# Kernel optimization log

Hardware: AMD Instinct MI355X
Metric: run time of the kernel (lower is better)

## Reference

```python
import jax, jax.numpy as jnp
import numpy as np
import math

EMBED = 512
KDIM = 512
VDIM = 512
H = 8
HD = EMBED // H
N = 2048
L = 2048
B = 4


def setup_inputs() -> dict:
    key = jax.random.key(0)
    ks = jax.random.split(key, 14)
    s = 1.0 / math.sqrt(EMBED)
    return {
        "q": jax.random.normal(ks[0], (N, B, EMBED), jnp.float32),
        "k": jax.random.normal(ks[1], (L, B, KDIM), jnp.float32),
        "v": jax.random.normal(ks[2], (L, B, VDIM), jnp.float32),
        "pe1": jax.random.normal(ks[3], (B, N, 3), jnp.float32),
        "pe2": jax.random.normal(ks[4], (L, 3), jnp.float32),
        "Wq": jax.random.normal(ks[5], (EMBED, EMBED), jnp.float32) * s,
        "bq": jnp.zeros((EMBED,), jnp.float32),
        "Wk": jax.random.normal(ks[6], (EMBED, KDIM), jnp.float32) * s,
        "bk": jnp.zeros((EMBED,), jnp.float32),
        "Wv": jax.random.normal(ks[7], (EMBED, VDIM), jnp.float32) * s,
        "bv": jnp.zeros((EMBED,), jnp.float32),
        "Wo": jax.random.normal(ks[8], (EMBED, EMBED), jnp.float32) * s,
        "bo": jnp.zeros((EMBED,), jnp.float32),
    }


def reference(q, k, v, pe1, pe2, Wq, bq, Wk, bk, Wv, bv, Wo, bo):
    n, b, _ = q.shape
    l = k.shape[0]
    # projections (nn.Linear: x @ W.T + b)
    qp = q @ Wq.T + bq  # (n, b, E)
    kp = k @ Wk.T + bk  # (l, b, E)
    vp = v @ Wv.T + bv  # (l, b, E)
    # split heads -> (b, H, n, hd)
    qh = qp.reshape(n, b, H, HD).transpose(1, 2, 0, 3)
    kh = kp.reshape(l, b, H, HD).transpose(1, 2, 0, 3)
    vh = vp.reshape(l, b, H, HD).transpose(1, 2, 0, 3)
    # relative PE bias: (b, n, l), broadcast over heads
    pe_scores = jnp.einsum('bnc,lc->bnl', pe1, pe2)[:, None, :, :]
    scores = (jnp.einsum('bhnd,bhld->bhnl', qh, kh) + pe_scores) / math.sqrt(HD)
    attn = jax.nn.softmax(scores, axis=-1)
    out = jnp.einsum('bhnl,bhld->bhnd', attn, vh)  # (b, H, n, hd)
    out = out.transpose(2, 0, 1, 3).reshape(n, b, EMBED)
    return out @ Wo.T + bo
```

## Files before the change

kernel.cpp:

```cpp
#include <hip/hip_runtime.h>
#include <math.h>

#define EMBED 512
#define HDIM 64
#define NHEADS 8
#define SEQ_N 2048
#define SEQ_L 2048
#define BATCH 4
#define MROWS (SEQ_N*BATCH)
#define BE (BATCH*EMBED)

#define QSCALE 0.18033688f

typedef _Float16 f16;
typedef _Float16 half8 __attribute__((ext_vector_type(8)));
typedef _Float16 half4 __attribute__((ext_vector_type(4)));
typedef float floatx4 __attribute__((ext_vector_type(4)));
typedef float floatx16 __attribute__((ext_vector_type(16)));

static __device__ inline float fast_exp2(float x) {
#if __has_builtin(__builtin_amdgcn_exp2f)
  return __builtin_amdgcn_exp2f(x);
#else
  return __expf(x * 0.69314718056f);
#endif
}

__global__ __launch_bounds__(256) void cvt_all(const float* __restrict__ q,
                                               const float* __restrict__ k,
                                               const float* __restrict__ v,
                                               const float* __restrict__ Wq,
                                               const float* __restrict__ Wk,
                                               const float* __restrict__ Wv,
                                               const float* __restrict__ Wo,
                                               f16* __restrict__ qb, f16* __restrict__ kb,
                                               f16* __restrict__ vb, f16* __restrict__ Wb) {
  const long TOK = (long)MROWS * EMBED;
  const long WSZ = (long)EMBED * EMBED;
  int y = blockIdx.y;
  long i = ((long)blockIdx.x * 256 + threadIdx.x) * 4;
  if (y < 3) {
    if (i < TOK) {
      const float* s = y == 0 ? q : y == 1 ? k : v;
      f16* d = y == 0 ? qb : y == 1 ? kb : vb;
      float4 f = *reinterpret_cast<const float4*>(s + i);
      half4 o; o[0] = (f16)f.x; o[1] = (f16)f.y; o[2] = (f16)f.z; o[3] = (f16)f.w;
      *reinterpret_cast<half4*>(d + i) = o;
    }
  } else {
    if (i < 4 * WSZ) {
      int sel = (int)(i >> 18);
      long off = i & (WSZ - 1);
      const float* s = sel == 0 ? Wq : sel == 1 ? Wk : sel == 2 ? Wv : Wo;
      float4 f = *reinterpret_cast<const float4*>(s + off);
      half4 o; o[0] = (f16)f.x; o[1] = (f16)f.y; o[2] = (f16)f.z; o[3] = (f16)f.w;
      *reinterpret_cast<half4*>(Wb + i) = o;
    }
  }
}

__global__ __launch_bounds__(256) void gemm_qkv(const f16* __restrict__ A0,
                                                const f16* __restrict__ A1,
                                                const f16* __restrict__ A2,
                                                const f16* __restrict__ W0,
                                                const f16* __restrict__ W1,
                                                const f16* __restrict__ W2,
                                                const float* __restrict__ b0,
                                                const float* __restrict__ b1,
                                                const float* __restrict__ b2,
                                                f16* __restrict__ C0, f16* __restrict__ C1,
                                                f16* __restrict__ C2t) {
  __shared__ alignas(16) f16 As[128 * 40];
  __shared__ alignas(16) f16 Bs[128 * 40];
  const int sel = blockIdx.y >> 2;
  const f16* A = sel == 0 ? A0 : sel == 1 ? A1 : A2;
  const f16* Bt = sel == 0 ? W0 : sel == 1 ? W1 : W2;
  const float* bias = sel == 0 ? b0 : sel == 1 ? b1 : b2;
  const float scl = sel == 0 ? QSCALE : 1.0f;
  const int tid = threadIdx.x;
  const int wave = tid >> 6, lane = tid & 63, quad = lane >> 4, l16 = lane & 15;
  const int wm = wave & 1, wn = wave >> 1;
  const long m0 = (long)blockIdx.x * 128;
  const long n0 = (long)(blockIdx.y & 3) * 128;
  floatx4 acc[4][4] = {};
  const int r0 = tid >> 2;
  const int c0 = (tid & 3) * 8;

  for (int k0 = 0; k0 < EMBED; k0 += 32) {
    __syncthreads();
    uint4 a0 = *reinterpret_cast<const uint4*>(A + (m0 + r0) * EMBED + k0 + c0);
    uint4 a1 = *reinterpret_cast<const uint4*>(A + (m0 + r0 + 64) * EMBED + k0 + c0);
    uint4 bb0 = *reinterpret_cast<const uint4*>(Bt + (n0 + r0) * EMBED + k0 + c0);
    uint4 bb1 = *reinterpret_cast<const uint4*>(Bt + (n0 + r0 + 64) * EMBED + k0 + c0);
    *reinterpret_cast<uint4*>(&As[r0 * 40 + c0]) = a0;
    *reinterpret_cast<uint4*>(&As[(r0 + 64) * 40 + c0]) = a1;
    *reinterpret_cast<uint4*>(&Bs[r0 * 40 + c0]) = bb0;
    *reinterpret_cast<uint4*>(&Bs[(r0 + 64) * 40 + c0]) = bb1;
    __syncthreads();
    half8 af[4], bf[4];
#pragma unroll
    for (int i = 0; i < 4; ++i)
      af[i] = *reinterpret_cast<const half8*>(&As[(wm * 64 + i * 16 + l16) * 40 + quad * 8]);
#pragma unroll
    for (int j = 0; j < 4; ++j)
      bf[j] = *reinterpret_cast<const half8*>(&Bs[(wn * 64 + j * 16 + l16) * 40 + quad * 8]);
#pragma unroll
    for (int i = 0; i < 4; ++i)
#pragma unroll
      for (int j = 0; j < 4; ++j)
        acc[i][j] = __builtin_amdgcn_mfma_f32_16x16x32_f16(af[i], bf[j], acc[i][j], 0, 0, 0);
  }
#pragma unroll
  for (int i = 0; i < 4; ++i)
#pragma unroll
    for (int r = 0; r < 4; ++r) {
      long row = m0 + wm * 64 + i * 16 + quad * 4 + r;
#pragma unroll
      for (int j = 0; j < 4; ++j) {
        long col = n0 + wn * 64 + j * 16 + l16;
        float val = (acc[i][j][r] + bias[col]) * scl;
        if (sel == 2) {
          long bq = row & 3, ltok = row >> 2;
          long hh = col >> 6, dd = col & 63;
          C2t[(((bq << 3) + hh) * 64 + dd) * 2048 + ltok] = (f16)val;
        } else {
          f16* C = sel == 0 ? C0 : C1;
          C[row * EMBED + col] = (f16)val;
        }
      }
    }
}

__global__ __launch_bounds__(256) void gemm_out(const f16* __restrict__ A,
                                                const f16* __restrict__ Bt,
                                                const float* __restrict__ bias,
                                                float* __restrict__ C) {
  __shared__ alignas(16) f16 As[128 * 40];
  __shared__ alignas(16) f16 Bs[64 * 40];
  const int tid = threadIdx.x;
  const int wave = tid >> 6, lane = tid & 63, quad = lane >> 4, l16 = lane & 15;
  const long m0 = (long)blockIdx.x * 128;
  const long n0 = (long)blockIdx.y * 64;
  floatx4 acc[2][4] = {};
  const int r0 = tid >> 2;
  const int c0 = (tid & 3) * 8;

  for (int k0 = 0; k0 < EMBED; k0 += 32) {
    __syncthreads();
    uint4 a0 = *reinterpret_cast<const uint4*>(A + (m0 + r0) * EMBED + k0 + c0);
    uint4 a1 = *reinterpret_cast<const uint4*>(A + (m0 + r0 + 64) * EMBED + k0 + c0);
    uint4 bb0 = *reinterpret_cast<const uint4*>(Bt + (n0 + r0) * EMBED + k0 + c0);
    *reinterpret_cast<uint4*>(&As[r0 * 40 + c0]) = a0;
    *reinterpret_cast<uint4*>(&As[(r0 + 64) * 40 + c0]) = a1;
    *reinterpret_cast<uint4*>(&Bs[r0 * 40 + c0]) = bb0;
    __syncthreads();
    half8 af[2], bf[4];
#pragma unroll
    for (int i = 0; i < 2; ++i)
      af[i] = *reinterpret_cast<const half8*>(&As[(wave * 32 + i * 16 + l16) * 40 + quad * 8]);
#pragma unroll
    for (int j = 0; j < 4; ++j)
      bf[j] = *reinterpret_cast<const half8*>(&Bs[(j * 16 + l16) * 40 + quad * 8]);
#pragma unroll
    for (int i = 0; i < 2; ++i)
#pragma unroll
      for (int j = 0; j < 4; ++j)
        acc[i][j] = __builtin_amdgcn_mfma_f32_16x16x32_f16(af[i], bf[j], acc[i][j], 0, 0, 0);
  }
#pragma unroll
  for (int i = 0; i < 2; ++i)
#pragma unroll
    for (int r = 0; r < 4; ++r) {
      long row = m0 + wave * 32 + i * 16 + quad * 4 + r;
#pragma unroll
      for (int j = 0; j < 4; ++j) {
        long col = n0 + j * 16 + l16;
        C[row * EMBED + col] = acc[i][j][r] + bias[col];
      }
    }
}

#define KST 88
#define VST 136
__global__ __launch_bounds__(256, 2) void attn_flash(const f16* __restrict__ qp,
                                                     const f16* __restrict__ kp,
                                                     const f16* __restrict__ vt,
                                                     const float* __restrict__ pe1,
                                                     const float* __restrict__ pe2,
                                                     f16* __restrict__ ao) {
  __shared__ alignas(16) f16 Qs[128 * KST];
  __shared__ alignas(16) f16 Ks[128 * KST];
  __shared__ alignas(16) f16 Vt[64 * VST];
  const int tid = threadIdx.x, wave = tid >> 6, lane = tid & 63;
  const int m = lane & 31, h = lane >> 5;
  const int n0 = blockIdx.x * 128;
  const int b = blockIdx.y >> 3, hd = blockIdx.y & 7;
  const long headoff = (long)b * EMBED + hd * HDIM;
  const long vhead = (long)blockIdx.y * 64 * 2048;

  for (int c = tid; c < 1024; c += 256) {
    int r = c >> 3, col = (c & 7) * 8;
    *reinterpret_cast<uint4*>(&Qs[r * KST + col]) =
        *reinterpret_cast<const uint4*>(qp + (long)(n0 + r) * BE + headoff + col);
  }
  const uint4 z4 = {0, 0, 0, 0};
  const uint2 z2 = {0, 0};
  for (int c = tid; c < 512; c += 256) {
    int r = c >> 2, s = c & 3;
    if (s == 0) *reinterpret_cast<uint2*>(&Qs[r * KST + 68]) = z2;
    else if (s == 1) *reinterpret_cast<uint4*>(&Qs[r * KST + 72]) = z4;
    else if (s == 2) *reinterpret_cast<uint4*>(&Qs[r * KST + 80]) = z4;
    if (s == 0) *reinterpret_cast<uint2*>(&Ks[r * KST + 68]) = z2;
    else if (s == 1) *reinterpret_cast<uint4*>(&Ks[r * KST + 72]) = z4;
    else if (s == 2) *reinterpret_cast<uint4*>(&Ks[r * KST + 80]) = z4;
  }
  if (tid < 128) {
    long base = ((long)b * SEQ_N + n0 + tid) * 3;
    half4 v8;
    v8[0] = (f16)(pe1[base + 0] * QSCALE);
    v8[1] = (f16)(pe1[base + 1] * QSCALE);
    v8[2] = (f16)(pe1[base + 2] * QSCALE);
    v8[3] = (f16)0.f;
    *reinterpret_cast<half4*>(&Qs[tid * KST + 64]) = v8;
  }
  __syncthreads();

  half8 qf[5];
#pragma unroll
  for (int e = 0; e < 5; ++e)
    qf[e] = *reinterpret_cast<const half8*>(&Qs[(wave * 32 + m) * KST + e * 16 + h * 8]);

  floatx16 oacc[2] = {};
  float lpart = 0.f;

  for (int l0 = 0; l0 < SEQ_L; l0 += 128) {
    __syncthreads();
    for (int c = tid; c < 1024; c += 256) {
      int r = c >> 3, col = (c & 7) * 8;
      *reinterpret_cast<uint4*>(&Ks[r * KST + col]) =
          *reinterpret_cast<const uint4*>(kp + (long)(l0 + r) * BE + headoff + col);
    }
    for (int c = tid; c < 1024; c += 256) {
      int r = c >> 4, col = (c & 15) * 8;
      *reinterpret_cast<uint4*>(&Vt[r * VST + col]) =
          *reinterpret_cast<const uint4*>(vt + vhead + (long)r * 2048 + l0 + col);
    }
    if (tid < 128) {
      long bb = (long)(l0 + tid) * 3;
      half4 p2;
      p2[0] = (f16)pe2[bb + 0];
      p2[1] = (f16)pe2[bb + 1];
      p2[2] = (f16)pe2[bb + 2];
      p2[3] = (f16)0.f;
      *reinterpret_cast<half4*>(&Ks[tid * KST + 64]) = p2;
    }
    __syncthreads();

#pragma unroll
    for (int t = 0; t < 4; ++t) {
      floatx16 st = {};
#pragma unroll
      for (int e = 0; e < 5; ++e) {
        half8 kf = *reinterpret_cast<const half8*>(&Ks[(t * 32 + m) * KST + e * 16 + h * 8]);
        st = __builtin_amdgcn_mfma_f32_32x32x16_f16(kf, qf[e], st, 0, 0, 0);
      }
      float p[16];
#pragma unroll
      for (int r = 0; r < 16; ++r) {
        p[r] = fast_exp2(st[r]);
        lpart += p[r];
      }
#pragma unroll
      for (int s = 0; s < 4; ++s) {
        half4 bp;
        bp[0] = (f16)p[4 * s + 0];
        bp[1] = (f16)p[4 * s + 1];
        bp[2] = (f16)p[4 * s + 2];
        bp[3] = (f16)p[4 * s + 3];
        int lcol = t * 32 + s * 8 + h * 4;
#pragma unroll
        for (int dt = 0; dt < 2; ++dt) {
          half4 vf = *reinterpret_cast<const half4*>(&Vt[(dt * 32 + m) * VST + lcol]);
          oacc[dt] = __builtin_amdgcn_mfma_f32_32x32x8f16(vf, bp, oacc[dt], 0, 0, 0);
        }
      }
    }
  }

  lpart += __shfl_xor(lpart, 32);
  float inv = 1.f / lpart;
  long qrow = n0 + wave * 32 + m;
#pragma unroll
  for (int dt = 0; dt < 2; ++dt)
#pragma unroll
    for (int g = 0; g < 4; ++g) {
      half4 o4;
      o4[0] = (f16)(oacc[dt][4 * g + 0] * inv);
      o4[1] = (f16)(oacc[dt][4 * g + 1] * inv);
      o4[2] = (f16)(oacc[dt][4 * g + 2] * inv);
      o4[3] = (f16)(oacc[dt][4 * g + 3] * inv);
      int d = dt * 32 + 8 * g + 4 * h;
      *reinterpret_cast<half4*>(ao + qrow * BE + headoff + d) = o4;
    }
}

extern "C" void kernel_launch(void* const* d_in, const int* in_sizes, int n_in,
                              void* d_out, int out_size, void* d_ws, size_t ws_size,
                              hipStream_t stream) {
  const float* q   = (const float*)d_in[0];
  const float* k   = (const float*)d_in[1];
  const float* v   = (const float*)d_in[2];
  const float* pe1 = (const float*)d_in[3];
  const float* pe2 = (const float*)d_in[4];
  const float* Wq  = (const float*)d_in[5];
  const float* bq  = (const float*)d_in[6];
  const float* Wk  = (const float*)d_in[7];
  const float* bk  = (const float*)d_in[8];
  const float* Wv  = (const float*)d_in[9];
  const float* bv  = (const float*)d_in[10];
  const float* Wo  = (const float*)d_in[11];
  const float* bo  = (const float*)d_in[12];
  float* out = (float*)d_out;

  f16* ws = (f16*)d_ws;
  const long TOK = (long)MROWS * EMBED;
  const long WSZ = (long)EMBED * EMBED;
  f16* qb  = ws;
  f16* kb  = qb + TOK;
  f16* vb  = kb + TOK;
  f16* Wqb = vb + TOK;
  f16* Wkb = Wqb + WSZ;
  f16* Wvb = Wkb + WSZ;
  f16* Wob = Wvb + WSZ;
  f16* qpb = Wob + WSZ;
  f16* kpb = qpb + TOK;
  f16* vtb = kpb + TOK;
  f16* aob = vtb + TOK;

  cvt_all<<<dim3(4096, 4), 256, 0, stream>>>(q, k, v, Wq, Wk, Wv, Wo, qb, kb, vb, Wqb);

  gemm_qkv<<<dim3(MROWS / 128, 12), 256, 0, stream>>>(qb, kb, vb, Wqb, Wkb, Wvb,
                                                      bq, bk, bv, qpb, kpb, vtb);

  attn_flash<<<dim3(SEQ_N / 128, BATCH * NHEADS), 256, 0, stream>>>(qpb, kpb, vtb, pe1, pe2, aob);

  gemm_out<<<dim3(MROWS / 128, EMBED / 64), 256, 0, stream>>>(aob, Wob, bo, out);
}
```

Baseline: 228.4 us.

## Fuse fp32-to-fp16 conversion into GEMM loads and prefetch K/V chunks in attention

Removes the separate conversion kernel. The QKV and output GEMMs now load fp32 inputs and weights directly and pack them to fp16 with cvt_pkrtz while staging into LDS, which saves one launch and a full write plus re-read of the converted tensors. The attention kernel register-prefetches the next K/V/pe2 chunk during compute (software pipelining), splits the output accumulators and the row-sum into two interleaved chains, and packs the probabilities with pkrtz. In exchange the GEMMs read twice the bytes per tile from global memory and repeat the conversion across tiles, the prefetch registers raise register pressure, and round-toward-zero conversion slightly changes numerics.

```diff
diff --git a/kernel.cpp b/kernel.cpp
--- a/kernel.cpp
+++ b/kernel.cpp
@@ -15,6 +15,7 @@
 typedef _Float16 f16;
 typedef _Float16 half8 __attribute__((ext_vector_type(8)));
 typedef _Float16 half4 __attribute__((ext_vector_type(4)));
+typedef _Float16 half2v __attribute__((ext_vector_type(2)));
 typedef float floatx4 __attribute__((ext_vector_type(4)));
 typedef float floatx16 __attribute__((ext_vector_type(16)));
 
@@ -26,45 +27,29 @@
 #endif
 }
 
-__global__ __launch_bounds__(256) void cvt_all(const float* __restrict__ q,
-                                               const float* __restrict__ k,
-                                               const float* __restrict__ v,
-                                               const float* __restrict__ Wq,
-                                               const float* __restrict__ Wk,
-                                               const float* __restrict__ Wv,
-                                               const float* __restrict__ Wo,
-                                               f16* __restrict__ qb, f16* __restrict__ kb,
-                                               f16* __restrict__ vb, f16* __restrict__ Wb) {
-  const long TOK = (long)MROWS * EMBED;
-  const long WSZ = (long)EMBED * EMBED;
-  int y = blockIdx.y;
-  long i = ((long)blockIdx.x * 256 + threadIdx.x) * 4;
-  if (y < 3) {
-    if (i < TOK) {
-      const float* s = y == 0 ? q : y == 1 ? k : v;
-      f16* d = y == 0 ? qb : y == 1 ? kb : vb;
-      float4 f = *reinterpret_cast<const float4*>(s + i);
-      half4 o; o[0] = (f16)f.x; o[1] = (f16)f.y; o[2] = (f16)f.z; o[3] = (f16)f.w;
-      *reinterpret_cast<half4*>(d + i) = o;
-    }
-  } else {
-    if (i < 4 * WSZ) {
-      int sel = (int)(i >> 18);
-      long off = i & (WSZ - 1);
-      const float* s = sel == 0 ? Wq : sel == 1 ? Wk : sel == 2 ? Wv : Wo;
-      float4 f = *reinterpret_cast<const float4*>(s + off);
-      half4 o; o[0] = (f16)f.x; o[1] = (f16)f.y; o[2] = (f16)f.z; o[3] = (f16)f.w;
-      *reinterpret_cast<half4*>(Wb + i) = o;
-    }
-  }
-}
-
-__global__ __launch_bounds__(256) void gemm_qkv(const f16* __restrict__ A0,
-                                                const f16* __restrict__ A1,
-                                                const f16* __restrict__ A2,
-                                                const f16* __restrict__ W0,
-                                                const f16* __restrict__ W1,
-                                                const f16* __restrict__ W2,
+static __device__ inline half2v pk2(float a, float b) {
+#if __has_builtin(__builtin_amdgcn_cvt_pkrtz)
+  return __builtin_bit_cast(half2v, __builtin_amdgcn_cvt_pkrtz(a, b));
+#else
+  half2v o; o[0] = (f16)a; o[1] = (f16)b; return o;
+#endif
+}
+
+static __device__ inline half8 cvt8(const float4& a, const float4& b) {
+  half2v p0 = pk2(a.x, a.y), p1 = pk2(a.z, a.w);
+  half2v p2 = pk2(b.x, b.y), p3 = pk2(b.z, b.w);
+  half8 o;
+  o[0] = p0[0]; o[1] = p0[1]; o[2] = p1[0]; o[3] = p1[1];
+  o[4] = p2[0]; o[5] = p2[1]; o[6] = p3[0]; o[7] = p3[1];
+  return o;
+}
+
+__global__ __launch_bounds__(256) void gemm_qkv(const float* __restrict__ A0,
+                                                const float* __restrict__ A1,
+                                                const float* __restrict__ A2,
+                                                const float* __restrict__ W0,
+                                                const float* __restrict__ W1,
+                                                const float* __restrict__ W2,
                                                 const float* __restrict__ b0,
                                                 const float* __restrict__ b1,
                                                 const float* __restrict__ b2,
@@ -73,8 +58,8 @@
   __shared__ alignas(16) f16 As[128 * 40];
   __shared__ alignas(16) f16 Bs[128 * 40];
   const int sel = blockIdx.y >> 2;
-  const f16* A = sel == 0 ? A0 : sel == 1 ? A1 : A2;
-  const f16* Bt = sel == 0 ? W0 : sel == 1 ? W1 : W2;
+  const float* A = sel == 0 ? A0 : sel == 1 ? A1 : A2;
+  const float* Bt = sel == 0 ? W0 : sel == 1 ? W1 : W2;
   const float* bias = sel == 0 ? b0 : sel == 1 ? b1 : b2;
   const float scl = sel == 0 ? QSCALE : 1.0f;
   const int tid = threadIdx.x;
@@ -88,14 +73,18 @@
 
   for (int k0 = 0; k0 < EMBED; k0 += 32) {
     __syncthreads();
-    uint4 a0 = *reinterpret_cast<const uint4*>(A + (m0 + r0) * EMBED + k0 + c0);
-    uint4 a1 = *reinterpret_cast<const uint4*>(A + (m0 + r0 + 64) * EMBED + k0 + c0);
-    uint4 bb0 = *reinterpret_cast<const uint4*>(Bt + (n0 + r0) * EMBED + k0 + c0);
-    uint4 bb1 = *reinterpret_cast<const uint4*>(Bt + (n0 + r0 + 64) * EMBED + k0 + c0);
-    *reinterpret_cast<uint4*>(&As[r0 * 40 + c0]) = a0;
-    *reinterpret_cast<uint4*>(&As[(r0 + 64) * 40 + c0]) = a1;
-    *reinterpret_cast<uint4*>(&Bs[r0 * 40 + c0]) = bb0;
-    *reinterpret_cast<uint4*>(&Bs[(r0 + 64) * 40 + c0]) = bb1;
+    float4 a00 = *reinterpret_cast<const float4*>(A + (m0 + r0) * EMBED + k0 + c0);
+    float4 a01 = *reinterpret_cast<const float4*>(A + (m0 + r0) * EMBED + k0 + c0 + 4);
+    float4 a10 = *reinterpret_cast<const float4*>(A + (m0 + r0 + 64) * EMBED + k0 + c0);
+    float4 a11 = *reinterpret_cast<const float4*>(A + (m0 + r0 + 64) * EMBED + k0 + c0 + 4);
+    float4 w00 = *reinterpret_cast<const float4*>(Bt + (n0 + r0) * EMBED + k0 + c0);
+    float4 w01 = *reinterpret_cast<const float4*>(Bt + (n0 + r0) * EMBED + k0 + c0 + 4);
+    float4 w10 = *reinterpret_cast<const float4*>(Bt + (n0 + r0 + 64) * EMBED + k0 + c0);
+    float4 w11 = *reinterpret_cast<const float4*>(Bt + (n0 + r0 + 64) * EMBED + k0 + c0 + 4);
+    *reinterpret_cast<half8*>(&As[r0 * 40 + c0]) = cvt8(a00, a01);
+    *reinterpret_cast<half8*>(&As[(r0 + 64) * 40 + c0]) = cvt8(a10, a11);
+    *reinterpret_cast<half8*>(&Bs[r0 * 40 + c0]) = cvt8(w00, w01);
+    *reinterpret_cast<half8*>(&Bs[(r0 + 64) * 40 + c0]) = cvt8(w10, w11);
     __syncthreads();
     half8 af[4], bf[4];
 #pragma unroll
@@ -132,7 +121,7 @@
 }
 
 __global__ __launch_bounds__(256) void gemm_out(const f16* __restrict__ A,
-                                                const f16* __restrict__ Bt,
+                                                const float* __restrict__ Wt,
                                                 const float* __restrict__ bias,
                                                 float* __restrict__ C) {
   __shared__ alignas(16) f16 As[128 * 40];
@@ -149,10 +138,11 @@
     __syncthreads();
     uint4 a0 = *reinterpret_cast<const uint4*>(A + (m0 + r0) * EMBED + k0 + c0);
     uint4 a1 = *reinterpret_cast<const uint4*>(A + (m0 + r0 + 64) * EMBED + k0 + c0);
-    uint4 bb0 = *reinterpret_cast<const uint4*>(Bt + (n0 + r0) * EMBED + k0 + c0);
+    float4 w0 = *reinterpret_cast<const float4*>(Wt + (n0 + r0) * EMBED + k0 + c0);
+    float4 w1 = *reinterpret_cast<const float4*>(Wt + (n0 + r0) * EMBED + k0 + c0 + 4);
     *reinterpret_cast<uint4*>(&As[r0 * 40 + c0]) = a0;
     *reinterpret_cast<uint4*>(&As[(r0 + 64) * 40 + c0]) = a1;
-    *reinterpret_cast<uint4*>(&Bs[r0 * 40 + c0]) = bb0;
+    *reinterpret_cast<half8*>(&Bs[r0 * 40 + c0]) = cvt8(w0, w1);
     __syncthreads();
     half8 af[2], bf[4];
 #pragma unroll
@@ -182,6 +172,7 @@
 
 #define KST 88
 #define VST 136
+#define NCHUNK (SEQ_L / 128)
 __global__ __launch_bounds__(256, 2) void attn_flash(const f16* __restrict__ qp,
                                                      const f16* __restrict__ kp,
                                                      const f16* __restrict__ vt,
@@ -223,39 +214,54 @@
     v8[3] = (f16)0.f;
     *reinterpret_cast<half4*>(&Qs[tid * KST + 64]) = v8;
   }
+
+  uint4 kr[4], vr[4];
+  float p2a = 0.f, p2b = 0.f, p2c = 0.f;
+  auto load_chunk = [&](int l0) {
+#pragma unroll
+    for (int i = 0; i < 4; ++i) {
+      int idx = tid + i * 256;
+      int r = idx >> 3, col = (idx & 7) * 8;
+      kr[i] = *reinterpret_cast<const uint4*>(kp + (long)(l0 + r) * BE + headoff + col);
+      int rv = idx >> 4, cv = (idx & 15) * 8;
+      vr[i] = *reinterpret_cast<const uint4*>(vt + vhead + (long)rv * 2048 + l0 + cv);
+    }
+    if (tid < 128) {
+      long bb = (long)(l0 + tid) * 3;
+      p2a = pe2[bb + 0]; p2b = pe2[bb + 1]; p2c = pe2[bb + 2];
+    }
+  };
+  auto store_chunk = [&]() {
+#pragma unroll
+    for (int i = 0; i < 4; ++i) {
+      int idx = tid + i * 256;
+      int r = idx >> 3, col = (idx & 7) * 8;
+      *reinterpret_cast<uint4*>(&Ks[r * KST + col]) = kr[i];
+      int rv = idx >> 4, cv = (idx & 15) * 8;
+      *reinterpret_cast<uint4*>(&Vt[rv * VST + cv]) = vr[i];
+    }
+    if (tid < 128) {
+      half4 p2;
+      p2[0] = (f16)p2a; p2[1] = (f16)p2b; p2[2] = (f16)p2c; p2[3] = (f16)0.f;
+      *reinterpret_cast<half4*>(&Ks[tid * KST + 64]) = p2;
+    }
+  };
+
+  load_chunk(0);
   __syncthreads();
-
   half8 qf[5];
 #pragma unroll
   for (int e = 0; e < 5; ++e)
     qf[e] = *reinterpret_cast<const half8*>(&Qs[(wave * 32 + m) * KST + e * 16 + h * 8]);
-
-  floatx16 oacc[2] = {};
-  float lpart = 0.f;
-
-  for (int l0 = 0; l0 < SEQ_L; l0 += 128) {
-    __syncthreads();
-    for (int c = tid; c < 1024; c += 256) {
-      int r = c >> 3, col = (c & 7) * 8;
-      *reinterpret_cast<uint4*>(&Ks[r * KST + col]) =
-          *reinterpret_cast<const uint4*>(kp + (long)(l0 + r) * BE + headoff + col);
-    }
-    for (int c = tid; c < 1024; c += 256) {
-      int r = c >> 4, col = (c & 15) * 8;
-      *reinterpret_cast<uint4*>(&Vt[r * VST + col]) =
-          *reinterpret_cast<const uint4*>(vt + vhead + (long)r * 2048 + l0 + col);
-    }
-    if (tid < 128) {
-      long bb = (long)(l0 + tid) * 3;
-      half4 p2;
-      p2[0] = (f16)pe2[bb + 0];
-      p2[1] = (f16)pe2[bb + 1];
-      p2[2] = (f16)pe2[bb + 2];
-      p2[3] = (f16)0.f;
-      *reinterpret_cast<half4*>(&Ks[tid * KST + 64]) = p2;
-    }
-    __syncthreads();
-
+  store_chunk();
+
+  floatx16 oacc[2][2] = {};
+  float lp0 = 0.f, lp1 = 0.f;
+
+#pragma unroll 1
+  for (int c = 0; c < NCHUNK; ++c) {
+    if (c + 1 < NCHUNK) load_chunk((c + 1) * 128);
+    __syncthreads();
 #pragma unroll
     for (int t = 0; t < 4; ++t) {
       floatx16 st = {};
@@ -266,27 +272,30 @@
       }
       float p[16];
 #pragma unroll
-      for (int r = 0; r < 16; ++r) {
-        p[r] = fast_exp2(st[r]);
-        lpart += p[r];
-      }
+      for (int r = 0; r < 16; ++r) p[r] = fast_exp2(st[r]);
+#pragma unroll
+      for (int r = 0; r < 16; r += 2) { lp0 += p[r]; lp1 += p[r + 1]; }
 #pragma unroll
       for (int s = 0; s < 4; ++s) {
+        half2v u0 = pk2(p[4 * s + 0], p[4 * s + 1]);
+        half2v u1 = pk2(p[4 * s + 2], p[4 * s + 3]);
         half4 bp;
-        bp[0] = (f16)p[4 * s + 0];
-        bp[1] = (f16)p[4 * s + 1];
-        bp[2] = (f16)p[4 * s + 2];
-        bp[3] = (f16)p[4 * s + 3];
+        bp[0] = u0[0]; bp[1] = u0[1]; bp[2] = u1[0]; bp[3] = u1[1];
         int lcol = t * 32 + s * 8 + h * 4;
 #pragma unroll
         for (int dt = 0; dt < 2; ++dt) {
           half4 vf = *reinterpret_cast<const half4*>(&Vt[(dt * 32 + m) * VST + lcol]);
-          oacc[dt] = __builtin_amdgcn_mfma_f32_32x32x8f16(vf, bp, oacc[dt], 0, 0, 0);
+          oacc[dt][t & 1] = __builtin_amdgcn_mfma_f32_32x32x8f16(vf, bp, oacc[dt][t & 1], 0, 0, 0);
         }
       }
     }
-  }
-
+    if (c + 1 < NCHUNK) {
+      __syncthreads();
+      store_chunk();
+    }
+  }
+
+  float lpart = lp0 + lp1;
   lpart += __shfl_xor(lpart, 32);
   float inv = 1.f / lpart;
   long qrow = n0 + wave * 32 + m;
@@ -295,10 +304,11 @@
 #pragma unroll
     for (int g = 0; g < 4; ++g) {
       half4 o4;
-      o4[0] = (f16)(oacc[dt][4 * g + 0] * inv);
-      o4[1] = (f16)(oacc[dt][4 * g + 1] * inv);
-      o4[2] = (f16)(oacc[dt][4 * g + 2] * inv);
-      o4[3] = (f16)(oacc[dt][4 * g + 3] * inv);
+#pragma unroll
+      for (int x = 0; x < 4; ++x) {
+        float o = oacc[dt][0][4 * g + x] + oacc[dt][1][4 * g + x];
+        o4[x] = (f16)(o * inv);
+      }
       int d = dt * 32 + 8 * g + 4 * h;
       *reinterpret_cast<half4*>(ao + qrow * BE + headoff + d) = o4;
     }
@@ -324,25 +334,15 @@
 
   f16* ws = (f16*)d_ws;
   const long TOK = (long)MROWS * EMBED;
-  const long WSZ = (long)EMBED * EMBED;
-  f16* qb  = ws;
-  f16* kb  = qb + TOK;
-  f16* vb  = kb + TOK;
-  f16* Wqb = vb + TOK;
-  f16* Wkb = Wqb + WSZ;
-  f16* Wvb = Wkb + WSZ;
-  f16* Wob = Wvb + WSZ;
-  f16* qpb = Wob + WSZ;
+  f16* qpb = ws;
   f16* kpb = qpb + TOK;
   f16* vtb = kpb + TOK;
   f16* aob = vtb + TOK;
 
-  cvt_all<<<dim3(4096, 4), 256, 0, stream>>>(q, k, v, Wq, Wk, Wv, Wo, qb, kb, vb, Wqb);
-
-  gemm_qkv<<<dim3(MROWS / 128, 12), 256, 0, stream>>>(qb, kb, vb, Wqb, Wkb, Wvb,
+  gemm_qkv<<<dim3(MROWS / 128, 12), 256, 0, stream>>>(q, k, v, Wq, Wk, Wv,
                                                       bq, bk, bv, qpb, kpb, vtb);
 
   attn_flash<<<dim3(SEQ_N / 128, BATCH * NHEADS), 256, 0, stream>>>(qpb, kpb, vtb, pe1, pe2, aob);
 
-  gemm_out<<<dim3(MROWS / 128, EMBED / 64), 256, 0, stream>>>(aob, Wob, bo, out);
-}
+  gemm_out<<<dim3(MROWS / 128, EMBED / 64), 256, 0, stream>>>(aob, Wo, bo, out);
+}
```

Result: slower. 251.1 us (+10.0%).
